# Kernel tuning notes

Measured on AMD Instinct MI355X. Metric: run time of the kernel, lower is better.

Reference implementation:

```python
import jax, jax.numpy as jnp
import numpy as np

H = 14
W_FULL = 14  # spatial width; rfft width = 8


def setup_inputs() -> dict:
    key = jax.random.key(0)
    k1, k2 = jax.random.split(key)
    B, N, C = 256, 196, 768
    x = jax.random.normal(k1, (B, N, C), dtype=jnp.float32)
    complex_weight = jax.random.normal(k2, (14, 8, C, 2), dtype=jnp.float32) * 0.02
    return {"x": x, "complex_weight": complex_weight}


def reference(x, complex_weight):
    B, N, C = x.shape
    Hs = Ws = int(np.sqrt(N))  # 14, static
    xg = x.reshape(B, Hs, Ws, C).astype(jnp.float32)
    # 2D real FFT over spatial dims, orthonormal -> (B, Hs, Ws//2+1, C) complex
    xf = jnp.fft.rfft2(xg, axes=(1, 2), norm="ortho")
    weight = complex_weight[..., 0] + 1j * complex_weight[..., 1]  # (Hs, Ws//2+1, C)
    xf = xf * weight
    out = jnp.fft.irfft2(xf, s=(Hs, Ws), axes=(1, 2), norm="ortho")
    return out.reshape(B, N, C)
```

## Files before the change

### kernel.cpp

```cpp
#include <hip/hip_runtime.h>
#include <hip/hip_bf16.h>


static constexpr int CB     = 64;
static constexpr int NT     = 512;
static constexpr int CTILES = 768 / CB;

static constexpr float C14[14] = {
     1.0f,
     0.90096886790241915f,  0.62348980185873359f,  0.22252093395631445f,
    -0.22252093395631434f, -0.62348980185873348f, -0.90096886790241915f,
    -1.0f,
    -0.90096886790241926f, -0.62348980185873371f, -0.22252093395631456f,
     0.22252093395631423f,  0.62348980185873337f,  0.90096886790241904f
};
static constexpr float S14[14] = {
     0.0f,
     0.43388373911755812f,  0.78183148246802980f,  0.97492791218182362f,
     0.97492791218182362f,  0.78183148246802991f,  0.43388373911755823f,
     0.0f,
    -0.43388373911755806f, -0.78183148246802958f, -0.97492791218182362f,
    -0.97492791218182373f, -0.78183148246802991f, -0.43388373911755834f
};

__device__ __forceinline__ uint32_t pk_bf16(float re, float im) {
    union { __hip_bfloat162 h2; uint32_t u; } cv;
    cv.h2 = __float22bfloat162_rn(make_float2(re, im));
    return cv.u;
}
__device__ __forceinline__ float2 up_bf16(uint32_t v) {
    return make_float2(__uint_as_float(v << 16),
                       __uint_as_float(v & 0xffff0000u));
}

__global__ __launch_bounds__(NT, 3) void gfnet_filter(
    const float* __restrict__ x,
    const float* __restrict__ wgt,
    float* __restrict__ out)
{
    __shared__ uint32_t T[14 * 8 * 64];

    const int bid = blockIdx.x;
    const int b   = bid / CTILES;
    const int ct  = bid - b * CTILES;
    const int c0  = ct * CB;
    const int tid = threadIdx.x;
    const int wv  = tid >> 6;
    const int ln  = tid & 63;
    const bool two = (wv < 6);
    const int r0 = wv;
    const int r1 = wv + 8;

    const float* xb = x + (size_t)b * 196 * 768 + c0 + ln;

    float A0r[8], A0i[7], A1r[8], A1i[7];
    {
        float v0[14], v1[14];
        #pragma unroll
        for (int w = 0; w < 14; ++w) v0[w] = xb[(size_t)(r0 * 14 + w) * 768];
        if (two) {
            #pragma unroll
            for (int w = 0; w < 14; ++w) v1[w] = xb[(size_t)(r1 * 14 + w) * 768];
        }
        {
            float s[7], d[7];
            #pragma unroll
            for (int j = 1; j <= 6; ++j) { s[j] = v0[j] + v0[14 - j]; d[j] = v0[j] - v0[14 - j]; }
            A0r[0] = v0[0] + v0[7] + s[1] + s[2] + s[3] + s[4] + s[5] + s[6];
            A0r[7] = v0[0] - v0[7] - s[1] + s[2] - s[3] + s[4] - s[5] + s[6];
            #pragma unroll
            for (int u = 1; u <= 6; ++u) {
                float re = (u & 1) ? (v0[0] - v0[7]) : (v0[0] + v0[7]);
                float im = 0.f;
                #pragma unroll
                for (int j = 1; j <= 6; ++j) {
                    re = fmaf(s[j],  C14[(u * j) % 14], re);
                    im = fmaf(d[j], -S14[(u * j) % 14], im);
                }
                A0r[u] = re; A0i[u] = im;
            }
        }
        if (two) {
            float s[7], d[7];
            #pragma unroll
            for (int j = 1; j <= 6; ++j) { s[j] = v1[j] + v1[14 - j]; d[j] = v1[j] - v1[14 - j]; }
            A1r[0] = v1[0] + v1[7] + s[1] + s[2] + s[3] + s[4] + s[5] + s[6];
            A1r[7] = v1[0] - v1[7] - s[1] + s[2] - s[3] + s[4] - s[5] + s[6];
            #pragma unroll
            for (int u = 1; u <= 6; ++u) {
                float re = (u & 1) ? (v1[0] - v1[7]) : (v1[0] + v1[7]);
                float im = 0.f;
                #pragma unroll
                for (int j = 1; j <= 6; ++j) {
                    re = fmaf(s[j],  C14[(u * j) % 14], re);
                    im = fmaf(d[j], -S14[(u * j) % 14], im);
                }
                A1r[u] = re; A1i[u] = im;
            }
        }
    }

    #pragma unroll
    for (int u = 0; u < 8; ++u)
        T[(r0 * 8 + u) * 64 + ln] =
            pk_bf16(A0r[u], (u >= 1 && u <= 6) ? A0i[u] : 0.f);
    if (two) {
        #pragma unroll
        for (int u = 0; u < 8; ++u)
            T[(r1 * 8 + u) * 64 + ln] =
                pk_bf16(A1r[u], (u >= 1 && u <= 6) ? A1i[u] : 0.f);
    }

    float wr[14], wi[14];
    {
        const float2* wb = reinterpret_cast<const float2*>(wgt) + (size_t)wv * 768 + c0 + ln;
        #pragma unroll
        for (int k = 0; k < 14; ++k) {
            const float2 t = wb[(size_t)k * (8 * 768)];
            wr[k] = t.x; wi[k] = t.y;
        }
    }

    __syncthreads();

    float gr[14], gi[14];
    #pragma unroll
    for (int h = 0; h < 14; ++h) {
        float2 t = up_bf16(T[(h * 8 + wv) * 64 + ln]);
        gr[h] = t.x; gi[h] = t.y;
    }

    float esr[3], esi[3], edr[3], edi[3], osr[3], osi[3], odr[3], odi[3];
    #pragma unroll
    for (int i = 0; i < 3; ++i) {
        int j = 2 * (i + 1);
        esr[i] = gr[j] + gr[14 - j]; esi[i] = gi[j] + gi[14 - j];
        edr[i] = gr[j] - gr[14 - j]; edi[i] = gi[j] - gi[14 - j];
        j = 2 * i + 1;
        osr[i] = gr[j] + gr[14 - j]; osi[i] = gi[j] + gi[14 - j];
        odr[i] = gr[j] - gr[14 - j]; odi[i] = gi[j] - gi[14 - j];
    }
    float Ekr[7], Eki[7], Okr[7], Oki[7];
    Ekr[0] = gr[0] + esr[0] + esr[1] + esr[2];
    Eki[0] = gi[0] + esi[0] + esi[1] + esi[2];
    Okr[0] = gr[7] + osr[0] + osr[1] + osr[2];
    Oki[0] = gi[7] + osi[0] + osi[1] + osi[2];
    #pragma unroll
    for (int k = 1; k <= 6; ++k) {
        float er = gr[0], ei = gi[0];
        #pragma unroll
        for (int i = 0; i < 3; ++i) {
            const int j = 2 * (i + 1);
            const float c = C14[(j * k) % 14], s2 = S14[(j * k) % 14];
            er = fmaf(esr[i], c, er); er = fmaf(edi[i],  s2, er);
            ei = fmaf(esi[i], c, ei); ei = fmaf(edr[i], -s2, ei);
        }
        Ekr[k] = er; Eki[k] = ei;
        float onr = (k & 1) ? -gr[7] : gr[7];
        float oni = (k & 1) ? -gi[7] : gi[7];
        #pragma unroll
        for (int i = 0; i < 3; ++i) {
            const int j = 2 * i + 1;
            const float c = C14[(j * k) % 14], s2 = S14[(j * k) % 14];
            onr = fmaf(osr[i], c, onr); onr = fmaf(odi[i],  s2, onr);
            oni = fmaf(osi[i], c, oni); oni = fmaf(odr[i], -s2, oni);
        }
        Okr[k] = onr; Oki[k] = oni;
    }

    float Hr[14], Hi[14];
    #pragma unroll
    for (int k = 0; k < 7; ++k) {
        const float ar = Ekr[k] + Okr[k], ai = Eki[k] + Oki[k];
        const float br = Ekr[k] - Okr[k], bi = Eki[k] - Oki[k];
        Hr[k]     = fmaf(ar, wr[k],     -(ai * wi[k]));
        Hi[k]     = fmaf(ar, wi[k],       ai * wr[k]);
        Hr[k + 7] = fmaf(br, wr[k + 7], -(bi * wi[k + 7]));
        Hi[k + 7] = fmaf(br, wi[k + 7],   bi * wr[k + 7]);
    }

    float qsr[3], qsi[3], qdr[3], qdi[3], rsr[3], rsi[3], rdr[3], rdi[3];
    #pragma unroll
    for (int i = 0; i < 3; ++i) {
        int j = 2 * (i + 1);
        qsr[i] = Hr[j] + Hr[14 - j]; qsi[i] = Hi[j] + Hi[14 - j];
        qdr[i] = Hr[j] - Hr[14 - j]; qdi[i] = Hi[j] - Hi[14 - j];
        j = 2 * i + 1;
        rsr[i] = Hr[j] + Hr[14 - j]; rsi[i] = Hi[j] + Hi[14 - j];
        rdr[i] = Hr[j] - Hr[14 - j]; rdi[i] = Hi[j] - Hi[14 - j];
    }
    float Qr[7], Qi[7], Rr[7], Ri[7];
    Qr[0] = Hr[0] + qsr[0] + qsr[1] + qsr[2];
    Qi[0] = Hi[0] + qsi[0] + qsi[1] + qsi[2];
    Rr[0] = Hr[7] + rsr[0] + rsr[1] + rsr[2];
    Ri[0] = Hi[7] + rsi[0] + rsi[1] + rsi[2];
    #pragma unroll
    for (int m = 1; m <= 6; ++m) {
        float qr = Hr[0], qi2 = Hi[0];
        #pragma unroll
        for (int i = 0; i < 3; ++i) {
            const int j = 2 * (i + 1);
            const float c = C14[(j * m) % 14], s2 = S14[(j * m) % 14];
            qr  = fmaf(qsr[i], c, qr);  qr  = fmaf(qdi[i], -s2, qr);
            qi2 = fmaf(qsi[i], c, qi2); qi2 = fmaf(qdr[i],  s2, qi2);
        }
        Qr[m] = qr; Qi[m] = qi2;
        float rr = (m & 1) ? -Hr[7] : Hr[7];
        float ri2 = (m & 1) ? -Hi[7] : Hi[7];
        #pragma unroll
        for (int i = 0; i < 3; ++i) {
            const int j = 2 * i + 1;
            const float c = C14[(j * m) % 14], s2 = S14[(j * m) % 14];
            rr  = fmaf(rsr[i], c, rr);  rr  = fmaf(rdi[i], -s2, rr);
            ri2 = fmaf(rsi[i], c, ri2); ri2 = fmaf(rdr[i],  s2, ri2);
        }
        Rr[m] = rr; Ri[m] = ri2;
    }

    __syncthreads();

    #pragma unroll
    for (int m = 0; m < 7; ++m) {
        T[(m * 8 + wv) * 64 + ln]       = pk_bf16(Qr[m] + Rr[m], Qi[m] + Ri[m]);
        T[((m + 7) * 8 + wv) * 64 + ln] = pk_bf16(Qr[m] - Rr[m], Qi[m] - Ri[m]);
    }
    __syncthreads();

    float* ob = out + (size_t)b * 196 * 768 + c0 + ln;
    #pragma unroll
    for (int rr = 0; rr < 2; ++rr) {
        const int row = rr ? r1 : r0;
        if (rr == 0 || two) {
            float a0[8], b0v[7];
            #pragma unroll
            for (int v = 0; v < 8; ++v) {
                float2 t = up_bf16(T[(row * 8 + v) * 64 + ln]);
                a0[v] = t.x * ((v == 0 || v == 7) ? (1.0f / 196.0f) : (2.0f / 196.0f));
                if (v >= 1 && v <= 6) b0v[v] = t.y * (2.0f / 196.0f);
            }
            ob[(size_t)(row * 14 + 0) * 768] = a0[0] + a0[7] + a0[1] + a0[2] + a0[3] + a0[4] + a0[5] + a0[6];
            ob[(size_t)(row * 14 + 7) * 768] = a0[0] - a0[7] - a0[1] + a0[2] - a0[3] + a0[4] - a0[5] + a0[6];
            #pragma unroll
            for (int wp = 1; wp <= 6; ++wp) {
                float t1 = (wp & 1) ? (a0[0] - a0[7]) : (a0[0] + a0[7]);
                float t2 = 0.f;
                #pragma unroll
                for (int v = 1; v <= 6; ++v) {
                    t1 = fmaf(a0[v],  C14[(v * wp) % 14], t1);
                    t2 = fmaf(b0v[v], S14[(v * wp) % 14], t2);
                }
                ob[(size_t)(row * 14 + wp) * 768]      = t1 - t2;
                ob[(size_t)(row * 14 + 14 - wp) * 768] = t1 + t2;
            }
        }
    }
}

extern "C" void kernel_launch(void* const* d_in, const int* in_sizes, int n_in,
                              void* d_out, int out_size, void* d_ws, size_t ws_size,
                              hipStream_t stream) {
    const float* x   = (const float*)d_in[0];
    const float* wgt = (const float*)d_in[1];
    float*       o   = (float*)d_out;

    const int B = in_sizes[0] / (196 * 768);
    dim3 grid(B * CTILES), block(NT);
    gfnet_filter<<<grid, block, 0, stream>>>(x, wgt, o);
}
```

Before: 69.05 us.

## Vectorize DFT stages with packed float2 FMA and use nontemporal output stores

Rewrites every DFT stage on 2-wide float vectors so the compiler can emit packed FP32 ops (v_pk_fma_f32). The two spatial rows per thread, or the real and imaginary parts, share one packed instruction, and the complex multiplies are restructured around swizzled operands. Output stores become nontemporal to avoid polluting cache. This targets ALU instruction count. The cost is extra lane-swizzle moves, and waves 6 and 7 now do redundant work on a zero-filled second row.

```diff
diff --git a/kernel.cpp b/kernel.cpp
--- a/kernel.cpp
+++ b/kernel.cpp
@@ -5,6 +5,8 @@
 static constexpr int CB     = 64;
 static constexpr int NT     = 512;
 static constexpr int CTILES = 768 / CB;
+
+typedef float f2 __attribute__((ext_vector_type(2)));
 
 static constexpr float C14[14] = {
      1.0f,
@@ -23,14 +25,19 @@
     -0.97492791218182373f, -0.78183148246802991f, -0.43388373911755834f
 };
 
+__device__ __forceinline__ f2 mk2(float a, float b) { f2 r; r.x = a; r.y = b; return r; }
+__device__ __forceinline__ f2 sp2(float a)          { f2 r; r.x = a; r.y = a; return r; }
+__device__ __forceinline__ f2 fma2(f2 a, float c, f2 acc) {
+    return __builtin_elementwise_fma(a, sp2(c), acc);
+}
+
 __device__ __forceinline__ uint32_t pk_bf16(float re, float im) {
     union { __hip_bfloat162 h2; uint32_t u; } cv;
     cv.h2 = __float22bfloat162_rn(make_float2(re, im));
     return cv.u;
 }
-__device__ __forceinline__ float2 up_bf16(uint32_t v) {
-    return make_float2(__uint_as_float(v << 16),
-                       __uint_as_float(v & 0xffff0000u));
+__device__ __forceinline__ f2 up_bf16(uint32_t v) {
+    return mk2(__uint_as_float(v << 16), __uint_as_float(v & 0xffff0000u));
 }
 
 __global__ __launch_bounds__(NT, 3) void gfnet_filter(
@@ -53,204 +60,193 @@
 
     const float* xb = x + (size_t)b * 196 * 768 + c0 + ln;
 
-    float A0r[8], A0i[7], A1r[8], A1i[7];
+    f2 Ar[8], Ai[7];
     {
-        float v0[14], v1[14];
-        #pragma unroll
-        for (int w = 0; w < 14; ++w) v0[w] = xb[(size_t)(r0 * 14 + w) * 768];
+        f2 v[14];
+        #pragma unroll
+        for (int w = 0; w < 14; ++w) {
+            v[w].x = xb[(size_t)(r0 * 14 + w) * 768];
+            v[w].y = 0.f;
+        }
         if (two) {
             #pragma unroll
-            for (int w = 0; w < 14; ++w) v1[w] = xb[(size_t)(r1 * 14 + w) * 768];
-        }
-        {
-            float s[7], d[7];
+            for (int w = 0; w < 14; ++w) v[w].y = xb[(size_t)(r1 * 14 + w) * 768];
+        }
+        f2 s[7], d[7];
+        #pragma unroll
+        for (int j = 1; j <= 6; ++j) { s[j] = v[j] + v[14 - j]; d[j] = v[j] - v[14 - j]; }
+        const f2 p = v[0] + v[7], q = v[0] - v[7];
+        Ar[0] = p + s[1] + s[2] + s[3] + s[4] + s[5] + s[6];
+        Ar[7] = q - s[1] + s[2] - s[3] + s[4] - s[5] + s[6];
+        #pragma unroll
+        for (int u = 1; u <= 6; ++u) {
+            f2 re = (u & 1) ? q : p;
+            f2 im = sp2(0.f);
             #pragma unroll
-            for (int j = 1; j <= 6; ++j) { s[j] = v0[j] + v0[14 - j]; d[j] = v0[j] - v0[14 - j]; }
-            A0r[0] = v0[0] + v0[7] + s[1] + s[2] + s[3] + s[4] + s[5] + s[6];
-            A0r[7] = v0[0] - v0[7] - s[1] + s[2] - s[3] + s[4] - s[5] + s[6];
-            #pragma unroll
-            for (int u = 1; u <= 6; ++u) {
-                float re = (u & 1) ? (v0[0] - v0[7]) : (v0[0] + v0[7]);
-                float im = 0.f;
-                #pragma unroll
-                for (int j = 1; j <= 6; ++j) {
-                    re = fmaf(s[j],  C14[(u * j) % 14], re);
-                    im = fmaf(d[j], -S14[(u * j) % 14], im);
-                }
-                A0r[u] = re; A0i[u] = im;
+            for (int j = 1; j <= 6; ++j) {
+                re = fma2(s[j],  C14[(u * j) % 14], re);
+                im = fma2(d[j], -S14[(u * j) % 14], im);
             }
-        }
-        if (two) {
-            float s[7], d[7];
-            #pragma unroll
-            for (int j = 1; j <= 6; ++j) { s[j] = v1[j] + v1[14 - j]; d[j] = v1[j] - v1[14 - j]; }
-            A1r[0] = v1[0] + v1[7] + s[1] + s[2] + s[3] + s[4] + s[5] + s[6];
-            A1r[7] = v1[0] - v1[7] - s[1] + s[2] - s[3] + s[4] - s[5] + s[6];
-            #pragma unroll
-            for (int u = 1; u <= 6; ++u) {
-                float re = (u & 1) ? (v1[0] - v1[7]) : (v1[0] + v1[7]);
-                float im = 0.f;
-                #pragma unroll
-                for (int j = 1; j <= 6; ++j) {
-                    re = fmaf(s[j],  C14[(u * j) % 14], re);
-                    im = fmaf(d[j], -S14[(u * j) % 14], im);
-                }
-                A1r[u] = re; A1i[u] = im;
-            }
+            Ar[u] = re; Ai[u] = im;
         }
     }
 
     #pragma unroll
     for (int u = 0; u < 8; ++u)
         T[(r0 * 8 + u) * 64 + ln] =
-            pk_bf16(A0r[u], (u >= 1 && u <= 6) ? A0i[u] : 0.f);
+            pk_bf16(Ar[u].x, (u >= 1 && u <= 6) ? Ai[u].x : 0.f);
     if (two) {
         #pragma unroll
         for (int u = 0; u < 8; ++u)
             T[(r1 * 8 + u) * 64 + ln] =
-                pk_bf16(A1r[u], (u >= 1 && u <= 6) ? A1i[u] : 0.f);
-    }
-
-    float wr[14], wi[14];
+                pk_bf16(Ar[u].y, (u >= 1 && u <= 6) ? Ai[u].y : 0.f);
+    }
+
+    f2 w2[14];
     {
         const float2* wb = reinterpret_cast<const float2*>(wgt) + (size_t)wv * 768 + c0 + ln;
         #pragma unroll
         for (int k = 0; k < 14; ++k) {
             const float2 t = wb[(size_t)k * (8 * 768)];
-            wr[k] = t.x; wi[k] = t.y;
+            w2[k] = mk2(t.x, t.y);
         }
     }
 
     __syncthreads();
 
-    float gr[14], gi[14];
-    #pragma unroll
-    for (int h = 0; h < 14; ++h) {
-        float2 t = up_bf16(T[(h * 8 + wv) * 64 + ln]);
-        gr[h] = t.x; gi[h] = t.y;
-    }
-
-    float esr[3], esi[3], edr[3], edi[3], osr[3], osi[3], odr[3], odi[3];
+    f2 g[14];
+    #pragma unroll
+    for (int h = 0; h < 14; ++h) g[h] = up_bf16(T[(h * 8 + wv) * 64 + ln]);
+
+    f2 es[3], eds[3], os[3], ods[3];
     #pragma unroll
     for (int i = 0; i < 3; ++i) {
         int j = 2 * (i + 1);
-        esr[i] = gr[j] + gr[14 - j]; esi[i] = gi[j] + gi[14 - j];
-        edr[i] = gr[j] - gr[14 - j]; edi[i] = gi[j] - gi[14 - j];
+        es[i] = g[j] + g[14 - j];
+        f2 ed = g[j] - g[14 - j];
+        eds[i] = mk2(ed.y, -ed.x);
         j = 2 * i + 1;
-        osr[i] = gr[j] + gr[14 - j]; osi[i] = gi[j] + gi[14 - j];
-        odr[i] = gr[j] - gr[14 - j]; odi[i] = gi[j] - gi[14 - j];
-    }
-    float Ekr[7], Eki[7], Okr[7], Oki[7];
-    Ekr[0] = gr[0] + esr[0] + esr[1] + esr[2];
-    Eki[0] = gi[0] + esi[0] + esi[1] + esi[2];
-    Okr[0] = gr[7] + osr[0] + osr[1] + osr[2];
-    Oki[0] = gi[7] + osi[0] + osi[1] + osi[2];
+        os[i] = g[j] + g[14 - j];
+        f2 od = g[j] - g[14 - j];
+        ods[i] = mk2(od.y, -od.x);
+    }
+    f2 E[7], O[7];
+    E[0] = g[0] + es[0] + es[1] + es[2];
+    O[0] = g[7] + os[0] + os[1] + os[2];
     #pragma unroll
     for (int k = 1; k <= 6; ++k) {
-        float er = gr[0], ei = gi[0];
+        f2 e = g[0];
         #pragma unroll
         for (int i = 0; i < 3; ++i) {
             const int j = 2 * (i + 1);
-            const float c = C14[(j * k) % 14], s2 = S14[(j * k) % 14];
-            er = fmaf(esr[i], c, er); er = fmaf(edi[i],  s2, er);
-            ei = fmaf(esi[i], c, ei); ei = fmaf(edr[i], -s2, ei);
-        }
-        Ekr[k] = er; Eki[k] = ei;
-        float onr = (k & 1) ? -gr[7] : gr[7];
-        float oni = (k & 1) ? -gi[7] : gi[7];
+            e = fma2(es[i],  C14[(j * k) % 14], e);
+            e = fma2(eds[i], S14[(j * k) % 14], e);
+        }
+        E[k] = e;
+        f2 o = (k & 1) ? -g[7] : g[7];
         #pragma unroll
         for (int i = 0; i < 3; ++i) {
             const int j = 2 * i + 1;
-            const float c = C14[(j * k) % 14], s2 = S14[(j * k) % 14];
-            onr = fmaf(osr[i], c, onr); onr = fmaf(odi[i],  s2, onr);
-            oni = fmaf(osi[i], c, oni); oni = fmaf(odr[i], -s2, oni);
-        }
-        Okr[k] = onr; Oki[k] = oni;
-    }
-
-    float Hr[14], Hi[14];
+            o = fma2(os[i],  C14[(j * k) % 14], o);
+            o = fma2(ods[i], S14[(j * k) % 14], o);
+        }
+        O[k] = o;
+    }
+
+    f2 H[14];
     #pragma unroll
     for (int k = 0; k < 7; ++k) {
-        const float ar = Ekr[k] + Okr[k], ai = Eki[k] + Oki[k];
-        const float br = Ekr[k] - Okr[k], bi = Eki[k] - Oki[k];
-        Hr[k]     = fmaf(ar, wr[k],     -(ai * wi[k]));
-        Hi[k]     = fmaf(ar, wi[k],       ai * wr[k]);
-        Hr[k + 7] = fmaf(br, wr[k + 7], -(bi * wi[k + 7]));
-        Hi[k + 7] = fmaf(br, wi[k + 7],   bi * wr[k + 7]);
-    }
-
-    float qsr[3], qsi[3], qdr[3], qdi[3], rsr[3], rsi[3], rdr[3], rdi[3];
+        const f2 a_ = E[k] + O[k];
+        const f2 b_ = E[k] - O[k];
+        const f2 wsA = mk2(-w2[k].y, w2[k].x);
+        const f2 wsB = mk2(-w2[k + 7].y, w2[k + 7].x);
+        H[k]     = __builtin_elementwise_fma(w2[k],     sp2(a_.x), wsA * sp2(a_.y));
+        H[k + 7] = __builtin_elementwise_fma(w2[k + 7], sp2(b_.x), wsB * sp2(b_.y));
+    }
+
+    f2 qs[3], qds[3], rs[3], rds[3];
     #pragma unroll
     for (int i = 0; i < 3; ++i) {
         int j = 2 * (i + 1);
-        qsr[i] = Hr[j] + Hr[14 - j]; qsi[i] = Hi[j] + Hi[14 - j];
-        qdr[i] = Hr[j] - Hr[14 - j]; qdi[i] = Hi[j] - Hi[14 - j];
+        qs[i] = H[j] + H[14 - j];
+        f2 qd = H[j] - H[14 - j];
+        qds[i] = mk2(-qd.y, qd.x);
         j = 2 * i + 1;
-        rsr[i] = Hr[j] + Hr[14 - j]; rsi[i] = Hi[j] + Hi[14 - j];
-        rdr[i] = Hr[j] - Hr[14 - j]; rdi[i] = Hi[j] - Hi[14 - j];
-    }
-    float Qr[7], Qi[7], Rr[7], Ri[7];
-    Qr[0] = Hr[0] + qsr[0] + qsr[1] + qsr[2];
-    Qi[0] = Hi[0] + qsi[0] + qsi[1] + qsi[2];
-    Rr[0] = Hr[7] + rsr[0] + rsr[1] + rsr[2];
-    Ri[0] = Hi[7] + rsi[0] + rsi[1] + rsi[2];
+        rs[i] = H[j] + H[14 - j];
+        f2 rd = H[j] - H[14 - j];
+        rds[i] = mk2(-rd.y, rd.x);
+    }
+    f2 Q[7], R[7];
+    Q[0] = H[0] + qs[0] + qs[1] + qs[2];
+    R[0] = H[7] + rs[0] + rs[1] + rs[2];
     #pragma unroll
     for (int m = 1; m <= 6; ++m) {
-        float qr = Hr[0], qi2 = Hi[0];
+        f2 qq = H[0];
         #pragma unroll
         for (int i = 0; i < 3; ++i) {
             const int j = 2 * (i + 1);
-            const float c = C14[(j * m) % 14], s2 = S14[(j * m) % 14];
-            qr  = fmaf(qsr[i], c, qr);  qr  = fmaf(qdi[i], -s2, qr);
-            qi2 = fmaf(qsi[i], c, qi2); qi2 = fmaf(qdr[i],  s2, qi2);
-        }
-        Qr[m] = qr; Qi[m] = qi2;
-        float rr = (m & 1) ? -Hr[7] : Hr[7];
-        float ri2 = (m & 1) ? -Hi[7] : Hi[7];
+            qq = fma2(qs[i],  C14[(j * m) % 14], qq);
+            qq = fma2(qds[i], S14[(j * m) % 14], qq);
+        }
+        Q[m] = qq;
+        f2 rr = (m & 1) ? -H[7] : H[7];
         #pragma unroll
         for (int i = 0; i < 3; ++i) {
             const int j = 2 * i + 1;
-            const float c = C14[(j * m) % 14], s2 = S14[(j * m) % 14];
-            rr  = fmaf(rsr[i], c, rr);  rr  = fmaf(rdi[i], -s2, rr);
-            ri2 = fmaf(rsi[i], c, ri2); ri2 = fmaf(rdr[i],  s2, ri2);
-        }
-        Rr[m] = rr; Ri[m] = ri2;
+            rr = fma2(rs[i],  C14[(j * m) % 14], rr);
+            rr = fma2(rds[i], S14[(j * m) % 14], rr);
+        }
+        R[m] = rr;
     }
 
     __syncthreads();
 
     #pragma unroll
     for (int m = 0; m < 7; ++m) {
-        T[(m * 8 + wv) * 64 + ln]       = pk_bf16(Qr[m] + Rr[m], Qi[m] + Ri[m]);
-        T[((m + 7) * 8 + wv) * 64 + ln] = pk_bf16(Qr[m] - Rr[m], Qi[m] - Ri[m]);
+        const f2 pa = Q[m] + R[m];
+        const f2 pb = Q[m] - R[m];
+        T[(m * 8 + wv) * 64 + ln]       = pk_bf16(pa.x, pa.y);
+        T[((m + 7) * 8 + wv) * 64 + ln] = pk_bf16(pb.x, pb.y);
     }
     __syncthreads();
 
     float* ob = out + (size_t)b * 196 * 768 + c0 + ln;
-    #pragma unroll
-    for (int rr = 0; rr < 2; ++rr) {
-        const int row = rr ? r1 : r0;
-        if (rr == 0 || two) {
-            float a0[8], b0v[7];
+    {
+        f2 a0[8], b0v[7];
+        #pragma unroll
+        for (int v = 0; v < 8; ++v) {
+            const f2 p0 = up_bf16(T[(r0 * 8 + v) * 64 + ln]);
+            f2 p1 = sp2(0.f);
+            if (two) p1 = up_bf16(T[(r1 * 8 + v) * 64 + ln]);
+            const float beta = (v == 0 || v == 7) ? (1.0f / 196.0f) : (2.0f / 196.0f);
+            a0[v] = mk2(p0.x, p1.x) * sp2(beta);
+            if (v >= 1 && v <= 6) b0v[v] = mk2(p0.y, p1.y) * sp2(2.0f / 196.0f);
+        }
+        const f2 pp = a0[0] + a0[7], qq = a0[0] - a0[7];
+        const f2 o0 = pp + a0[1] + a0[2] + a0[3] + a0[4] + a0[5] + a0[6];
+        const f2 o7 = qq - a0[1] + a0[2] - a0[3] + a0[4] - a0[5] + a0[6];
+        __builtin_nontemporal_store(o0.x, &ob[(size_t)(r0 * 14 + 0) * 768]);
+        __builtin_nontemporal_store(o7.x, &ob[(size_t)(r0 * 14 + 7) * 768]);
+        if (two) {
+            __builtin_nontemporal_store(o0.y, &ob[(size_t)(r1 * 14 + 0) * 768]);
+            __builtin_nontemporal_store(o7.y, &ob[(size_t)(r1 * 14 + 7) * 768]);
+        }
+        #pragma unroll
+        for (int wp = 1; wp <= 6; ++wp) {
+            f2 t1 = (wp & 1) ? qq : pp;
+            f2 t2 = sp2(0.f);
             #pragma unroll
-            for (int v = 0; v < 8; ++v) {
-                float2 t = up_bf16(T[(row * 8 + v) * 64 + ln]);
-                a0[v] = t.x * ((v == 0 || v == 7) ? (1.0f / 196.0f) : (2.0f / 196.0f));
-                if (v >= 1 && v <= 6) b0v[v] = t.y * (2.0f / 196.0f);
+            for (int v = 1; v <= 6; ++v) {
+                t1 = fma2(a0[v],  C14[(v * wp) % 14], t1);
+                t2 = fma2(b0v[v], S14[(v * wp) % 14], t2);
             }
-            ob[(size_t)(row * 14 + 0) * 768] = a0[0] + a0[7] + a0[1] + a0[2] + a0[3] + a0[4] + a0[5] + a0[6];
-            ob[(size_t)(row * 14 + 7) * 768] = a0[0] - a0[7] - a0[1] + a0[2] - a0[3] + a0[4] - a0[5] + a0[6];
-            #pragma unroll
-            for (int wp = 1; wp <= 6; ++wp) {
-                float t1 = (wp & 1) ? (a0[0] - a0[7]) : (a0[0] + a0[7]);
-                float t2 = 0.f;
-                #pragma unroll
-                for (int v = 1; v <= 6; ++v) {
-                    t1 = fmaf(a0[v],  C14[(v * wp) % 14], t1);
-                    t2 = fmaf(b0v[v], S14[(v * wp) % 14], t2);
-                }
-                ob[(size_t)(row * 14 + wp) * 768]      = t1 - t2;
-                ob[(size_t)(row * 14 + 14 - wp) * 768] = t1 + t2;
+            const f2 om = t1 - t2;
+            const f2 op = t1 + t2;
+            __builtin_nontemporal_store(om.x, &ob[(size_t)(r0 * 14 + wp) * 768]);
+            __builtin_nontemporal_store(op.x, &ob[(size_t)(r0 * 14 + 14 - wp) * 768]);
+            if (two) {
+                __builtin_nontemporal_store(om.y, &ob[(size_t)(r1 * 14 + wp) * 768]);
+                __builtin_nontemporal_store(op.y, &ob[(size_t)(r1 * 14 + 14 - wp) * 768]);
             }
         }
     }
```

Result: faster. 58.80 us (-14.8%).
